# Kernel tuning notes

Hardware: AMD Instinct MI355X
Metric: run time of the kernel (lower is better)

Reference implementation:

```python
import jax, jax.numpy as jnp
import numpy as np

TAU = 1.0
M_OUT = 32  # max_out_node_size
NEG = -1e30


def setup_inputs() -> dict:
    key = jax.random.key(0)
    B, H, U, maxN = 64, 512, 512, 512
    M = M_OUT
    in_size = H + M - 1
    lengths_np = np.where(np.arange(B) % 2 == 0, 256, 512).astype(np.int32)
    total = int(lengths_np.sum())  # 24576
    ks = jax.random.split(key, 14)
    h = jax.random.normal(ks[0], (total, H), jnp.float32)
    hg = jax.random.normal(ks[1], (B, H), jnp.float32)
    u = jax.random.uniform(ks[2], (M, B, maxN), jnp.float32, 1e-20, 1.0)
    gumbel = -jnp.log(-jnp.log(u))
    s = lambda k, shp, fan: jax.random.normal(k, shp, jnp.float32) * (fan ** -0.5)
    return {
        'h': h, 'hg': hg,
        'lengths': jnp.asarray(lengths_np),
        'gumbel': gumbel,
        'W1': s(ks[3], (U, H), H),
        'W2': s(ks[4], (U, H), H),
        'wc': s(ks[5], (U, 1), 1),
        'v': s(ks[6], (1, U), U),
        'w_ih': s(ks[7], (3 * H, in_size), in_size),
        'w_hh': s(ks[8], (3 * H, H), H),
        'b_ih': s(ks[9], (3 * H,), in_size),
        'b_hh': s(ks[10], (3 * H,), in_size),
        'Wf': s(ks[11], (M - 1, H), H),
        'bf': s(ks[12], (M - 1,), H),
    }


def _gru_cell(x, hprev, w_ih, w_hh, b_ih, b_hh):
    H = hprev.shape[-1]
    gi = x @ w_ih.T + b_ih
    gh = hprev @ w_hh.T + b_hh
    r = jax.nn.sigmoid(gi[:, :H] + gh[:, :H])
    z = jax.nn.sigmoid(gi[:, H:2 * H] + gh[:, H:2 * H])
    n = jnp.tanh(gi[:, 2 * H:] + r * gh[:, 2 * H:])
    return (1.0 - z) * n + z * hprev


def reference(h, hg, lengths, gumbel, W1, W2, wc, v, w_ih, w_hh, b_ih, b_hh, Wf, bf):
    B = lengths.shape[0]
    M, _, maxN = gumbel.shape
    H = hg.shape[1]
    total = h.shape[0]
    # pad_sequence: ragged h -> [B, maxN, H], zero-padded
    offsets = jnp.concatenate([jnp.zeros((1,), lengths.dtype), jnp.cumsum(lengths)[:-1]])
    pos = jnp.arange(maxN)
    mask = pos[None, :] < lengths[:, None]                      # [B, maxN]
    idx = jnp.clip(offsets[:, None] + pos[None, :], 0, total - 1)
    enc = h[idx] * mask[..., None].astype(h.dtype)              # [B, maxN, H]
    enc_proj = jnp.einsum('bnh,uh->bnu', enc, W1)               # W1(encoder_out), hoisted
    wc_vec = wc[:, 0]
    v_vec = v[0]
    theta_pos = jnp.arange(M - 1)

    def step(carry, xs):
        dec_in, hid, cov, closs = carry
        g, i = xs
        hid = _gru_cell(dec_in, hid, w_ih, w_hh, b_ih, b_hh)
        uj = jnp.tanh(enc_proj + (hid @ W2.T)[:, None, :] + cov[:, :, None] * wc_vec)
        scores = jnp.einsum('bnu,u->bn', uj, v_vec)
        att = jax.nn.softmax(jnp.where(mask, scores, NEG), axis=-1)  # [B, maxN]
        closs = closs + jnp.minimum(att, cov).sum()
        cov = cov + att
        # gumbel-softmax (hard, straight-through) over nodes
        y = jax.nn.softmax((jnp.log(att + 1e-12) + g) / TAU, axis=1)
        y_hard = jax.nn.one_hot(jnp.argmax(y, axis=1), maxN, dtype=y.dtype)
        att_hard = y_hard + y - jax.lax.stop_gradient(y)
        chosen = jnp.einsum('bnh,bn->bh', enc, att_hard)
        theta = jax.nn.sigmoid(hid @ Wf.T + bf) * (theta_pos < i).astype(hid.dtype)
        dec_in = jnp.concatenate([chosen, theta], axis=1)
        return (dec_in, hid, cov, closs), (att_hard, theta)

    dec_in0 = jnp.zeros((B, H + M - 1), h.dtype)
    cov0 = jnp.zeros((B, maxN), h.dtype)
    carry0 = (dec_in0, hg, cov0, jnp.asarray(0.0, h.dtype))
    (_, _, _, closs), (ptrs, thetas) = jax.lax.scan(step, carry0, (gumbel, jnp.arange(M)))
    pointer = jnp.transpose(ptrs, (1, 2, 0))   # [B, maxN, M]
    adj = jnp.transpose(thetas, (1, 2, 0))     # [B, M-1, M]
    return pointer, closs / B, enc, adj
```

## Files before the change

### kernel.cpp

```cpp
#include <hip/hip_runtime.h>
#include <math.h>

#define B 64
#define H 512
#define MAXN 512
#define U 512
#define MM 32
#define IN_SZ 543
#define DEC_STRIDE 544

#define PTR_OFF 0
#define PTR_SZ (B*MAXN*MM)
#define CLOSS_OFF (PTR_OFF + PTR_SZ)
#define ENC_OFF (CLOSS_OFF + 1)
#define ENC_SZ (B*MAXN*H)
#define ADJ_OFF (ENC_OFF + ENC_SZ)

#define EP_OFF 0
#define EP_SZ (B*MAXN*U)
#define GP_OFF (EP_OFF + EP_SZ)
#define GP_SZ (4*3*B*H)
#define HID0_OFF (GP_OFF + GP_SZ)
#define HID1_OFF (HID0_OFF + B*H)
#define W2H_OFF  (HID1_OFF + B*H)
#define COV_OFF  (W2H_OFF + B*H)
#define SC_OFF   (COV_OFF + B*MAXN)
#define DEC_OFF  (SC_OFF + B*MAXN)
#define CL_OFF   (DEC_OFF + B*DEC_STRIDE)
#define OFFS_OFF (CL_OFF + 64)

__device__ __forceinline__ float tanh_fast(float x){
    float e = __builtin_amdgcn_exp2f(x * 2.885390081777927f);
    return 1.0f - 2.0f * __builtin_amdgcn_rcpf(e + 1.0f);
}

__global__ void k_init(float* __restrict__ ws, float* __restrict__ out,
                       const float* __restrict__ hg, const int* __restrict__ lengths){
    int gid = blockIdx.x*256 + threadIdx.x;
    int nth = gridDim.x*256;
    float* ptr = out + PTR_OFF;
    for (int i=gid;i<PTR_SZ;i+=nth) ptr[i]=0.f;
    float* dec = ws + DEC_OFF;
    for (int i=gid;i<B*DEC_STRIDE;i+=nth) dec[i]=0.f;
    float* cov = ws + COV_OFF;
    float* hid0 = ws + HID0_OFF;
    for (int i=gid;i<B*H;i+=nth){ cov[i]=0.f; hid0[i]=hg[i]; }
    if (gid<64) (ws+CL_OFF)[gid]=0.f;
    if (gid==0){
        int* offs=(int*)(ws+OFFS_OFF); int acc=0;
        for(int b=0;b<B;b++){ offs[b]=acc; acc+=lengths[b]; }
    }
}

__global__ __launch_bounds__(256) void k_gather(const float* __restrict__ h,
        const int* __restrict__ lengths, const float* __restrict__ offs_f,
        float* __restrict__ enc){
    const int* offs = (const int*)offs_f;
    int t = threadIdx.x;
    int row = blockIdx.x*2 + (t>>7);
    int c = (t&127)*4;
    int b = row >> 9, n = row & 511;
    int len = lengths[b];
    float4 v = make_float4(0.f,0.f,0.f,0.f);
    if (n < len){
        const float* p = h + (size_t)(offs[b]+n)*H + c;
        v = *(const float4*)p;
    }
    float* q = enc + (size_t)row*H + c;
    q[0]=v.x; q[1]=v.y; q[2]=v.z; q[3]=v.w;
}

__global__ __launch_bounds__(256) void k_gemm_ep(const float* __restrict__ enc,
        const float* __restrict__ W1, float* __restrict__ ep){
    __shared__ float As[16][132];
    __shared__ float Bs[16][132];
    int tid = threadIdx.x;
    int bm = blockIdx.x >> 2, bn = blockIdx.x & 3;
    int r0 = bm*128, u0 = bn*128;
    int ty = tid >> 4, tx = tid & 15;
    float acc[8][8];
#pragma unroll
    for (int i=0;i<8;i++){
#pragma unroll
        for(int j=0;j<8;j++) acc[i][j]=0.f;
    }
    for (int k0=0;k0<512;k0+=16){
#pragma unroll
        for (int it=0; it<8; ++it){
            int idx = tid + it*256;
            int row = idx >> 4, k = idx & 15;
            As[k][row] = enc[(size_t)(r0+row)*512 + k0 + k];
        }
#pragma unroll
        for (int it=0; it<2; ++it){
            int idx = tid + it*256;
            int nn = idx >> 2, c = idx & 3;
            float4 v = *(const float4*)&W1[(size_t)(u0+nn)*512 + k0 + c*4];
            Bs[c*4+0][nn]=v.x; Bs[c*4+1][nn]=v.y; Bs[c*4+2][nn]=v.z; Bs[c*4+3][nn]=v.w;
        }
        __syncthreads();
#pragma unroll
        for (int k=0;k<16;k++){
            float4 a0 = *(const float4*)&As[k][ty*8];
            float4 a1 = *(const float4*)&As[k][ty*8+4];
            float4 b0 = *(const float4*)&Bs[k][tx*4];
            float4 b1 = *(const float4*)&Bs[k][64+tx*4];
            float a[8]={a0.x,a0.y,a0.z,a0.w,a1.x,a1.y,a1.z,a1.w};
            float bb[8]={b0.x,b0.y,b0.z,b0.w,b1.x,b1.y,b1.z,b1.w};
#pragma unroll
            for(int im=0;im<8;im++){
#pragma unroll
                for(int jn=0;jn<8;jn++) acc[im][jn] += a[im]*bb[jn];
            }
        }
        __syncthreads();
    }
#pragma unroll
    for (int im=0;im<8;im++){
        int r = r0 + ty*8 + im;
        float4 v0 = make_float4(acc[im][0],acc[im][1],acc[im][2],acc[im][3]);
        float4 v1 = make_float4(acc[im][4],acc[im][5],acc[im][6],acc[im][7]);
        *(float4*)&ep[(size_t)r*512 + u0 + tx*4] = v0;
        *(float4*)&ep[(size_t)r*512 + u0 + 64 + tx*4] = v1;
    }
}

__global__ __launch_bounds__(256) void k_gruP(const float* __restrict__ dec_in,
        const float* __restrict__ hid_in,
        const float* __restrict__ w_ih, const float* __restrict__ w_hh,
        float* __restrict__ gp){
    __shared__ float As[64][36];
    __shared__ float Ws[12][36];
    int tid=threadIdx.x, b=tid&63, q=tid>>6;
    int s = blockIdx.x >> 7;
    int h0 = (int)(blockIdx.x & 127) * 4;
    const float* xs; int xstride, kbeg, kend; const float* W; int wstride;
    if (s==0){ xs=dec_in; xstride=DEC_STRIDE; kbeg=0;   kend=288;   W=w_ih; wstride=IN_SZ; }
    else if(s==1){ xs=dec_in; xstride=DEC_STRIDE; kbeg=288; kend=IN_SZ; W=w_ih; wstride=IN_SZ; }
    else if(s==2){ xs=hid_in; xstride=512; kbeg=0;   kend=256; W=w_hh; wstride=512; }
    else         { xs=hid_in; xstride=512; kbeg=256; kend=512; W=w_hh; wstride=512; }
    float a0=0.f,a1=0.f,a2=0.f;
    for (int k0=kbeg; k0<kend; k0+=32){
        for (int it=0;it<2;it++){
            int idx=tid+it*256; int row=idx>>3, c=idx&7; int k=k0+c*4;
            float4 v=make_float4(0.f,0.f,0.f,0.f);
            const float* p=&xs[row*xstride+k];
            if (k+3 < kend) v=*(const float4*)p;
            else { if(k<kend)v.x=p[0]; if(k+1<kend)v.y=p[1]; if(k+2<kend)v.z=p[2]; }
            *(float4*)&As[row][c*4]=v;
        }
        if (tid<96){
            int rr=tid>>3, c=tid&7; int g=rr>>2, qq=rr&3;
            int j=g*512 + h0+qq; int k=k0+c*4;
            float4 v=make_float4(0.f,0.f,0.f,0.f);
            const float* p=&W[(size_t)j*wstride+k];
            if (wstride==512){
                v=*(const float4*)p;
            } else {
                if(k<kend)v.x=p[0]; if(k+1<kend)v.y=p[1];
                if(k+2<kend)v.z=p[2]; if(k+3<kend)v.w=p[3];
            }
            *(float4*)&Ws[rr][c*4]=v;
        }
        __syncthreads();
#pragma unroll
        for (int kk=0;kk<32;kk+=4){
            float4 a=*(const float4*)&As[b][kk];
            float4 w0=*(const float4*)&Ws[q][kk];
            float4 w1=*(const float4*)&Ws[4+q][kk];
            float4 w2=*(const float4*)&Ws[8+q][kk];
            a0 += a.x*w0.x + a.y*w0.y + a.z*w0.z + a.w*w0.w;
            a1 += a.x*w1.x + a.y*w1.y + a.z*w1.z + a.w*w1.w;
            a2 += a.x*w2.x + a.y*w2.y + a.z*w2.z + a.w*w2.w;
        }
        __syncthreads();
    }
    int h = h0 + q;
    gp[((s*3+0)*64+b)*512 + h] = a0;
    gp[((s*3+1)*64+b)*512 + h] = a1;
    gp[((s*3+2)*64+b)*512 + h] = a2;
}

__global__ __launch_bounds__(512) void k_mid(const float* __restrict__ gp,
        const float* __restrict__ hid_in, float* __restrict__ hid_out,
        const float* __restrict__ b_ih, const float* __restrict__ b_hh,
        const float* __restrict__ W2, const float* __restrict__ Wf,
        const float* __restrict__ bf,
        float* __restrict__ w2h, float* __restrict__ dec_in,
        float* __restrict__ adj, int step){
    __shared__ float sH[512];
    int b = blockIdx.x >> 2, uc = blockIdx.x & 3;
    int tid = threadIdx.x;
    {
        int h = tid;
        float gI0 = gp[((0*3+0)*64+b)*512+h] + gp[((1*3+0)*64+b)*512+h];
        float gI1 = gp[((0*3+1)*64+b)*512+h] + gp[((1*3+1)*64+b)*512+h];
        float gI2 = gp[((0*3+2)*64+b)*512+h] + gp[((1*3+2)*64+b)*512+h];
        float gH0 = gp[((2*3+0)*64+b)*512+h] + gp[((3*3+0)*64+b)*512+h];
        float gH1 = gp[((2*3+1)*64+b)*512+h] + gp[((3*3+1)*64+b)*512+h];
        float gH2 = gp[((2*3+2)*64+b)*512+h] + gp[((3*3+2)*64+b)*512+h];
        float gi0=gI0+b_ih[h],     gh0=gH0+b_hh[h];
        float gi1=gI1+b_ih[512+h], gh1=gH1+b_hh[512+h];
        float gi2=gI2+b_ih[1024+h],gh2=gH2+b_hh[1024+h];
        float r=1.f/(1.f+expf(-(gi0+gh0)));
        float z=1.f/(1.f+expf(-(gi1+gh1)));
        float nn=tanhf(gi2 + r*gh2);
        float hv=(1.f-z)*nn + z*hid_in[b*512+h];
        sH[h]=hv;
        if (uc==0) hid_out[b*512+h]=hv;
    }
    __syncthreads();
    int wv=tid>>6, lane=tid&63;
    for (int ul=wv; ul<128; ul+=8){
        int u = uc*128 + ul;
        const float* wr = &W2[(size_t)u*512];
        float acc=0.f;
#pragma unroll
        for (int t=0;t<8;t++){ int k=t*64+lane; acc += wr[k]*sH[k]; }
#pragma unroll
        for (int m=1;m<64;m<<=1) acc += __shfl_xor(acc, m, 64);
        if (lane==0) w2h[b*512+u]=acc;
    }
    if (uc==0){
        for (int ul=wv; ul<31; ul+=8){
            const float* wr = &Wf[(size_t)ul*512];
            float acc=0.f;
#pragma unroll
            for (int t=0;t<8;t++){ int k=t*64+lane; acc += wr[k]*sH[k]; }
#pragma unroll
            for (int m=1;m<64;m<<=1) acc += __shfl_xor(acc, m, 64);
            if (lane==0){
                float th = 1.f/(1.f+expf(-(acc + bf[ul])));
                th = (ul < step) ? th : 0.f;
                dec_in[b*DEC_STRIDE + 512 + ul] = th;
                adj[b*992 + ul*32 + step] = th;
            }
        }
    }
}

__global__ __launch_bounds__(256) void k_scores(const float* __restrict__ ep,
        const float* __restrict__ w2h, const float* __restrict__ cov,
        const float* __restrict__ wc, const float* __restrict__ v,
        const int* __restrict__ lengths, float* __restrict__ sc){
    __shared__ float sW[512], sV[512], sC[512];
    int b = blockIdx.x >> 4, nc = blockIdx.x & 15;
    int len = lengths[b];
    if (nc*32 >= len) return;
    int tid=threadIdx.x;
    for (int idx=tid; idx<384; idx+=256){
        int which = idx>>7, c = (idx&127)*4;
        float4 val;
        if (which==0) val=*(const float4*)&w2h[b*512+c];
        else if (which==1) val=*(const float4*)&v[c];
        else val=*(const float4*)&wc[c];
        float* dst = (which==0)?sW:((which==1)?sV:sC);
        *(float4*)&dst[c]=val;
    }
    __syncthreads();
    int wv=tid>>6, lane=tid&63;
    float4 vv0=*(const float4*)&sV[lane*8], vv1=*(const float4*)&sV[lane*8+4];
    float4 cc0=*(const float4*)&sC[lane*8], cc1=*(const float4*)&sC[lane*8+4];
    float4 ww0=*(const float4*)&sW[lane*8], ww1=*(const float4*)&sW[lane*8+4];
#pragma unroll
    for (int r=0;r<8;r++){
        int n = nc*32 + wv*8 + r;
        float cb = cov[b*512+n];
        const float4* rr = (const float4*)&ep[((size_t)b*512+n)*512 + lane*8];
        float4 e0=rr[0], e1=rr[1];
        float acc;
        acc  = tanh_fast(e0.x + ww0.x + cb*cc0.x)*vv0.x;
        acc += tanh_fast(e0.y + ww0.y + cb*cc0.y)*vv0.y;
        acc += tanh_fast(e0.z + ww0.z + cb*cc0.z)*vv0.z;
        acc += tanh_fast(e0.w + ww0.w + cb*cc0.w)*vv0.w;
        acc += tanh_fast(e1.x + ww1.x + cb*cc1.x)*vv1.x;
        acc += tanh_fast(e1.y + ww1.y + cb*cc1.y)*vv1.y;
        acc += tanh_fast(e1.z + ww1.z + cb*cc1.z)*vv1.z;
        acc += tanh_fast(e1.w + ww1.w + cb*cc1.w)*vv1.w;
#pragma unroll
        for (int m=1;m<64;m<<=1) acc += __shfl_xor(acc, m, 64);
        if (lane==0) sc[b*512+n]=acc;
    }
}

__global__ __launch_bounds__(512) void k_soft(const float* __restrict__ sc,
        const float* __restrict__ gum, const int* __restrict__ lengths,
        const float* __restrict__ enc, float* __restrict__ cov,
        float* __restrict__ dec_in, float* __restrict__ closs_b,
        float* __restrict__ pointer, int step){
    __shared__ float red[512];
    __shared__ int  redi[512];
    int b=blockIdx.x, n=threadIdx.x;
    int len=lengths[b];
    float e = (n<len)? expf(sc[b*512+n]) : 0.f;
    red[n]=e; __syncthreads();
    for(int o=256;o>=1;o>>=1){ if(n<o) red[n]+=red[n+o]; __syncthreads(); }
    float Z=red[0]; __syncthreads();
    float att=e/Z;
    float c=cov[b*512+n];
    red[n]=fminf(att,c); __syncthreads();
    for(int o=256;o>=1;o>>=1){ if(n<o) red[n]+=red[n+o]; __syncthreads(); }
    if(n==0) closs_b[b]+=red[0];
    __syncthreads();
    cov[b*512+n]=c+att;
    float lg=logf(att+1e-12f)+gum[((size_t)step*64+b)*512+n];
    red[n]=lg; redi[n]=n; __syncthreads();
    for(int o=256;o>=1;o>>=1){
        if(n<o && red[n+o]>red[n]){ red[n]=red[n+o]; redi[n]=redi[n+o]; }
        __syncthreads();
    }
    int ns=redi[0];
    if(n==0) pointer[b*16384 + ns*32 + step]=1.f;
    dec_in[b*DEC_STRIDE+n]=enc[((size_t)b*512+ns)*512+n];
}

__global__ void k_final(const float* __restrict__ closs_b, float* __restrict__ out){
    if (threadIdx.x==0 && blockIdx.x==0){
        float s=0.f;
        for(int b=0;b<B;b++) s+=closs_b[b];
        out[CLOSS_OFF]=s/64.f;
    }
}

extern "C" void kernel_launch(void* const* d_in, const int* in_sizes, int n_in,
                              void* d_out, int out_size, void* d_ws, size_t ws_size,
                              hipStream_t stream){
    const float* h      = (const float*)d_in[0];
    const float* hg     = (const float*)d_in[1];
    const int*   lengths= (const int*)  d_in[2];
    const float* gumbel = (const float*)d_in[3];
    const float* W1     = (const float*)d_in[4];
    const float* W2     = (const float*)d_in[5];
    const float* wc     = (const float*)d_in[6];
    const float* v      = (const float*)d_in[7];
    const float* w_ih   = (const float*)d_in[8];
    const float* w_hh   = (const float*)d_in[9];
    const float* b_ih   = (const float*)d_in[10];
    const float* b_hh   = (const float*)d_in[11];
    const float* Wf     = (const float*)d_in[12];
    const float* bf     = (const float*)d_in[13];
    float* out = (float*)d_out;
    float* ws  = (float*)d_ws;
    float* enc = out + ENC_OFF;
    float* adj = out + ADJ_OFF;
    float* pointer = out + PTR_OFF;
    float* ep   = ws + EP_OFF;
    float* gp   = ws + GP_OFF;
    float* hidA = ws + HID0_OFF;
    float* hidB = ws + HID1_OFF;
    float* w2h  = ws + W2H_OFF;
    float* cov  = ws + COV_OFF;
    float* sc   = ws + SC_OFF;
    float* dec  = ws + DEC_OFF;
    float* clb  = ws + CL_OFF;

    hipLaunchKernelGGL(k_init,   dim3(512),  dim3(256), 0, stream, ws, out, hg, lengths);
    hipLaunchKernelGGL(k_gather, dim3(16384),dim3(256), 0, stream, h, lengths, ws+OFFS_OFF, enc);
    hipLaunchKernelGGL(k_gemm_ep,dim3(1024), dim3(256), 0, stream, enc, W1, ep);

    for (int i=0;i<MM;i++){
        const float* hin = (i&1)? hidB : hidA;
        float*       hout= (i&1)? hidA : hidB;
        hipLaunchKernelGGL(k_gruP,   dim3(512),  dim3(256), 0, stream,
                           dec, hin, w_ih, w_hh, gp);
        hipLaunchKernelGGL(k_mid,    dim3(256),  dim3(512), 0, stream,
                           gp, hin, hout, b_ih, b_hh, W2, Wf, bf, w2h, dec, adj, i);
        hipLaunchKernelGGL(k_scores, dim3(1024), dim3(256), 0, stream,
                           ep, w2h, cov, wc, v, lengths, sc);
        hipLaunchKernelGGL(k_soft,   dim3(64),   dim3(512), 0, stream,
                           sc, gumbel, lengths, enc, cov, dec, clb, pointer, i);
    }
    hipLaunchKernelGGL(k_final, dim3(1), dim3(64), 0, stream, clb, out);
}
```

Baseline: 1.848 ms.

## Fuse per-step GRU tail, scoring and softmax into one kernel; MFMA encoder projection

Result: slower. 2.555 ms (+38.2%).

```diff
diff --git a/kernel.cpp b/kernel.cpp
--- a/kernel.cpp
+++ b/kernel.cpp
@@ -22,20 +22,29 @@
 #define GP_SZ (4*3*B*H)
 #define HID0_OFF (GP_OFF + GP_SZ)
 #define HID1_OFF (HID0_OFF + B*H)
-#define W2H_OFF  (HID1_OFF + B*H)
-#define COV_OFF  (W2H_OFF + B*H)
-#define SC_OFF   (COV_OFF + B*MAXN)
-#define DEC_OFF  (SC_OFF + B*MAXN)
+#define COV_OFF  (HID1_OFF + B*H)
+#define DEC_OFF  (COV_OFF + B*MAXN)
 #define CL_OFF   (DEC_OFF + B*DEC_STRIDE)
 #define OFFS_OFF (CL_OFF + 64)
+#define W2T_OFF  (OFFS_OFF + 64)
+
+typedef short bf16x8 __attribute__((ext_vector_type(8)));
+typedef float f32x4  __attribute__((ext_vector_type(4)));
 
 __device__ __forceinline__ float tanh_fast(float x){
     float e = __builtin_amdgcn_exp2f(x * 2.885390081777927f);
     return 1.0f - 2.0f * __builtin_amdgcn_rcpf(e + 1.0f);
 }
 
+__device__ __forceinline__ unsigned short f2bf(float x){
+    unsigned int u = __float_as_uint(x);
+    u = (u + 0x7fffu + ((u >> 16) & 1u)) >> 16;
+    return (unsigned short)u;
+}
+
 __global__ void k_init(float* __restrict__ ws, float* __restrict__ out,
-                       const float* __restrict__ hg, const int* __restrict__ lengths){
+                       const float* __restrict__ hg, const int* __restrict__ lengths,
+                       const float* __restrict__ W2){
     int gid = blockIdx.x*256 + threadIdx.x;
     int nth = gridDim.x*256;
     float* ptr = out + PTR_OFF;
@@ -45,6 +54,11 @@
     float* cov = ws + COV_OFF;
     float* hid0 = ws + HID0_OFF;
     for (int i=gid;i<B*H;i+=nth){ cov[i]=0.f; hid0[i]=hg[i]; }
+    float* w2t = ws + W2T_OFF;
+    for (int i=gid;i<512*512;i+=nth){
+        int u = i >> 9, k = i & 511;
+        w2t[k*512 + u] = W2[i];
+    }
     if (gid<64) (ws+CL_OFF)[gid]=0.f;
     if (gid==0){
         int* offs=(int*)(ws+OFFS_OFF); int acc=0;
@@ -70,58 +84,86 @@
     q[0]=v.x; q[1]=v.y; q[2]=v.z; q[3]=v.w;
 }
 
-__global__ __launch_bounds__(256) void k_gemm_ep(const float* __restrict__ enc,
+__global__ __launch_bounds__(256) void k_gemm_mfma(const float* __restrict__ enc,
         const float* __restrict__ W1, float* __restrict__ ep){
-    __shared__ float As[16][132];
-    __shared__ float Bs[16][132];
+    __shared__ unsigned short sAH[128][40];
+    __shared__ unsigned short sAL[128][40];
+    __shared__ unsigned short sBH[128][40];
+    __shared__ unsigned short sBL[128][40];
     int tid = threadIdx.x;
     int bm = blockIdx.x >> 2, bn = blockIdx.x & 3;
     int r0 = bm*128, u0 = bn*128;
-    int ty = tid >> 4, tx = tid & 15;
-    float acc[8][8];
-#pragma unroll
-    for (int i=0;i<8;i++){
-#pragma unroll
-        for(int j=0;j<8;j++) acc[i][j]=0.f;
-    }
-    for (int k0=0;k0<512;k0+=16){
-#pragma unroll
-        for (int it=0; it<8; ++it){
-            int idx = tid + it*256;
-            int row = idx >> 4, k = idx & 15;
-            As[k][row] = enc[(size_t)(r0+row)*512 + k0 + k];
-        }
-#pragma unroll
-        for (int it=0; it<2; ++it){
-            int idx = tid + it*256;
-            int nn = idx >> 2, c = idx & 3;
-            float4 v = *(const float4*)&W1[(size_t)(u0+nn)*512 + k0 + c*4];
-            Bs[c*4+0][nn]=v.x; Bs[c*4+1][nn]=v.y; Bs[c*4+2][nn]=v.z; Bs[c*4+3][nn]=v.w;
+    int wid = tid>>6, lane = tid&63;
+    int wr = wid>>1, wc = wid&1;
+    int lr = lane&15, lk = (lane>>4)*8;
+    f32x4 acc[4][4];
+#pragma unroll
+    for (int i=0;i<4;i++)
+#pragma unroll
+        for (int j=0;j<4;j++) acc[i][j] = (f32x4){0.f,0.f,0.f,0.f};
+    int rowA = tid>>2, seg = tid&3;
+    for (int k0=0;k0<512;k0+=32){
+#pragma unroll
+        for (int half=0; half<2; ++half){
+            int row = rowA + half*64;
+            const float* asrc = &enc[(size_t)(r0+row)*512 + k0 + seg*8];
+            bf16x8 vh, vl;
+#pragma unroll
+            for (int j=0;j<8;j++){
+                float x = asrc[j];
+                unsigned short hb = f2bf(x);
+                float hf = __uint_as_float(((unsigned int)hb)<<16);
+                vh[j] = (short)hb;
+                vl[j] = (short)f2bf(x - hf);
+            }
+            *(bf16x8*)&sAH[row][seg*8] = vh;
+            *(bf16x8*)&sAL[row][seg*8] = vl;
+            const float* bsrc = &W1[(size_t)(u0+row)*512 + k0 + seg*8];
+            float4 b0 = *(const float4*)bsrc;
+            float4 b1 = *(const float4*)(bsrc+4);
+            float xb[8] = {b0.x,b0.y,b0.z,b0.w,b1.x,b1.y,b1.z,b1.w};
+            bf16x8 wh, wl;
+#pragma unroll
+            for (int j=0;j<8;j++){
+                unsigned short hb = f2bf(xb[j]);
+                float hf = __uint_as_float(((unsigned int)hb)<<16);
+                wh[j] = (short)hb;
+                wl[j] = (short)f2bf(xb[j] - hf);
+            }
+            *(bf16x8*)&sBH[row][seg*8] = wh;
+            *(bf16x8*)&sBL[row][seg*8] = wl;
         }
         __syncthreads();
-#pragma unroll
-        for (int k=0;k<16;k++){
-            float4 a0 = *(const float4*)&As[k][ty*8];
-            float4 a1 = *(const float4*)&As[k][ty*8+4];
-            float4 b0 = *(const float4*)&Bs[k][tx*4];
-            float4 b1 = *(const float4*)&Bs[k][64+tx*4];
-            float a[8]={a0.x,a0.y,a0.z,a0.w,a1.x,a1.y,a1.z,a1.w};
-            float bb[8]={b0.x,b0.y,b0.z,b0.w,b1.x,b1.y,b1.z,b1.w};
-#pragma unroll
-            for(int im=0;im<8;im++){
-#pragma unroll
-                for(int jn=0;jn<8;jn++) acc[im][jn] += a[im]*bb[jn];
+        bf16x8 aH[4], aL[4], bH[4], bL[4];
+#pragma unroll
+        for (int f=0; f<4; f++){
+            aH[f] = *(const bf16x8*)&sAH[wr*64+f*16+lr][lk];
+            aL[f] = *(const bf16x8*)&sAL[wr*64+f*16+lr][lk];
+            bH[f] = *(const bf16x8*)&sBH[wc*64+f*16+lr][lk];
+            bL[f] = *(const bf16x8*)&sBL[wc*64+f*16+lr][lk];
+        }
+#pragma unroll
+        for (int mf=0;mf<4;mf++){
+#pragma unroll
+            for (int nf=0;nf<4;nf++){
+                acc[mf][nf] = __builtin_amdgcn_mfma_f32_16x16x32_bf16(aH[mf], bH[nf], acc[mf][nf], 0,0,0);
+                acc[mf][nf] = __builtin_amdgcn_mfma_f32_16x16x32_bf16(aH[mf], bL[nf], acc[mf][nf], 0,0,0);
+                acc[mf][nf] = __builtin_amdgcn_mfma_f32_16x16x32_bf16(aL[mf], bH[nf], acc[mf][nf], 0,0,0);
             }
         }
         __syncthreads();
     }
 #pragma unroll
-    for (int im=0;im<8;im++){
-        int r = r0 + ty*8 + im;
-        float4 v0 = make_float4(acc[im][0],acc[im][1],acc[im][2],acc[im][3]);
-        float4 v1 = make_float4(acc[im][4],acc[im][5],acc[im][6],acc[im][7]);
-        *(float4*)&ep[(size_t)r*512 + u0 + tx*4] = v0;
-        *(float4*)&ep[(size_t)r*512 + u0 + 64 + tx*4] = v1;
+    for (int mf=0;mf<4;mf++){
+#pragma unroll
+        for (int nf=0;nf<4;nf++){
+#pragma unroll
+            for (int r=0;r<4;r++){
+                int row = r0 + wr*64 + mf*16 + (lane>>4)*4 + r;
+                int col = u0 + wc*64 + nf*16 + lr;
+                ep[(size_t)row*512 + col] = acc[mf][nf][r];
+            }
+        }
     }
 }
 
@@ -181,17 +223,27 @@
     gp[((s*3+2)*64+b)*512 + h] = a2;
 }
 
-__global__ __launch_bounds__(512) void k_mid(const float* __restrict__ gp,
-        const float* __restrict__ hid_in, float* __restrict__ hid_out,
+__global__ __launch_bounds__(1024) void k_ss(
+        const float* __restrict__ gp, const float* __restrict__ hid_in,
+        float* __restrict__ hid_out,
         const float* __restrict__ b_ih, const float* __restrict__ b_hh,
-        const float* __restrict__ W2, const float* __restrict__ Wf,
-        const float* __restrict__ bf,
-        float* __restrict__ w2h, float* __restrict__ dec_in,
+        const float* __restrict__ w2t, const float* __restrict__ Wf,
+        const float* __restrict__ bf_,
+        const float* __restrict__ wc, const float* __restrict__ v,
+        const float* __restrict__ ep, const float* __restrict__ gum,
+        const int* __restrict__ lengths, const float* __restrict__ enc,
+        float* __restrict__ cov, float* __restrict__ dec_in,
+        float* __restrict__ clb, float* __restrict__ pointer,
         float* __restrict__ adj, int step){
-    __shared__ float sH[512];
-    int b = blockIdx.x >> 2, uc = blockIdx.x & 3;
-    int tid = threadIdx.x;
-    {
+    __shared__ float sH[512], sV[512], sC[512], sCov[512];
+    __shared__ float sWa[512], sWb[512], sW[512], sSc[512];
+    __shared__ float red[512];
+    __shared__ int  redi[512];
+    const int b = blockIdx.x, tid = threadIdx.x;
+    const int wv = tid>>6, lane = tid&63;
+    const int len = lengths[b];
+
+    if (tid < 512){
         int h = tid;
         float gI0 = gp[((0*3+0)*64+b)*512+h] + gp[((1*3+0)*64+b)*512+h];
         float gI1 = gp[((0*3+1)*64+b)*512+h] + gp[((1*3+1)*64+b)*512+h];
@@ -199,119 +251,108 @@
         float gH0 = gp[((2*3+0)*64+b)*512+h] + gp[((3*3+0)*64+b)*512+h];
         float gH1 = gp[((2*3+1)*64+b)*512+h] + gp[((3*3+1)*64+b)*512+h];
         float gH2 = gp[((2*3+2)*64+b)*512+h] + gp[((3*3+2)*64+b)*512+h];
-        float gi0=gI0+b_ih[h],     gh0=gH0+b_hh[h];
-        float gi1=gI1+b_ih[512+h], gh1=gH1+b_hh[512+h];
-        float gi2=gI2+b_ih[1024+h],gh2=gH2+b_hh[1024+h];
+        float gi0=gI0+b_ih[h],      gh0=gH0+b_hh[h];
+        float gi1=gI1+b_ih[512+h],  gh1=gH1+b_hh[512+h];
+        float gi2=gI2+b_ih[1024+h], gh2=gH2+b_hh[1024+h];
         float r=1.f/(1.f+expf(-(gi0+gh0)));
         float z=1.f/(1.f+expf(-(gi1+gh1)));
         float nn=tanhf(gi2 + r*gh2);
         float hv=(1.f-z)*nn + z*hid_in[b*512+h];
         sH[h]=hv;
-        if (uc==0) hid_out[b*512+h]=hv;
-    }
-    __syncthreads();
-    int wv=tid>>6, lane=tid&63;
-    for (int ul=wv; ul<128; ul+=8){
-        int u = uc*128 + ul;
-        const float* wr = &W2[(size_t)u*512];
-        float acc=0.f;
-#pragma unroll
-        for (int t=0;t<8;t++){ int k=t*64+lane; acc += wr[k]*sH[k]; }
-#pragma unroll
-        for (int m=1;m<64;m<<=1) acc += __shfl_xor(acc, m, 64);
-        if (lane==0) w2h[b*512+u]=acc;
-    }
-    if (uc==0){
-        for (int ul=wv; ul<31; ul+=8){
-            const float* wr = &Wf[(size_t)ul*512];
-            float acc=0.f;
-#pragma unroll
-            for (int t=0;t<8;t++){ int k=t*64+lane; acc += wr[k]*sH[k]; }
+        hid_out[b*512+h]=hv;
+    } else {
+        int t2 = tid - 512;
+        if (t2 < 128)      *(float4*)&sV[t2*4]         = *(const float4*)&v[t2*4];
+        else if (t2 < 256) *(float4*)&sC[(t2-128)*4]   = *(const float4*)&wc[(t2-128)*4];
+        else if (t2 < 384) *(float4*)&sCov[(t2-256)*4] = *(const float4*)&cov[b*512+(t2-256)*4];
+    }
+    __syncthreads();
+
+    {
+        int u = tid & 511;
+        int kb = (tid < 512) ? 0 : 256;
+        float acc = 0.f;
+#pragma unroll 8
+        for (int k=0;k<256;k++) acc += sH[kb+k] * w2t[(size_t)(kb+k)*512 + u];
+        if (tid < 512) sWa[u]=acc; else sWb[u]=acc;
+    }
+    __syncthreads();
+
+    if (tid < 512) sW[tid] = sWa[tid] + sWb[tid];
+    if (wv == 15){
+        float4 h0 = *(const float4*)&sH[lane*8];
+        float4 h1 = *(const float4*)&sH[lane*8+4];
+        for (int u=0; u<31; ++u){
+            const float4* wr_ = (const float4*)&Wf[(size_t)u*512 + lane*8];
+            float4 w0=wr_[0], w1=wr_[1];
+            float acc = w0.x*h0.x + w0.y*h0.y + w0.z*h0.z + w0.w*h0.w
+                      + w1.x*h1.x + w1.y*h1.y + w1.z*h1.z + w1.w*h1.w;
 #pragma unroll
             for (int m=1;m<64;m<<=1) acc += __shfl_xor(acc, m, 64);
             if (lane==0){
-                float th = 1.f/(1.f+expf(-(acc + bf[ul])));
-                th = (ul < step) ? th : 0.f;
-                dec_in[b*DEC_STRIDE + 512 + ul] = th;
-                adj[b*992 + ul*32 + step] = th;
-            }
-        }
-    }
-}
-
-__global__ __launch_bounds__(256) void k_scores(const float* __restrict__ ep,
-        const float* __restrict__ w2h, const float* __restrict__ cov,
-        const float* __restrict__ wc, const float* __restrict__ v,
-        const int* __restrict__ lengths, float* __restrict__ sc){
-    __shared__ float sW[512], sV[512], sC[512];
-    int b = blockIdx.x >> 4, nc = blockIdx.x & 15;
-    int len = lengths[b];
-    if (nc*32 >= len) return;
-    int tid=threadIdx.x;
-    for (int idx=tid; idx<384; idx+=256){
-        int which = idx>>7, c = (idx&127)*4;
-        float4 val;
-        if (which==0) val=*(const float4*)&w2h[b*512+c];
-        else if (which==1) val=*(const float4*)&v[c];
-        else val=*(const float4*)&wc[c];
-        float* dst = (which==0)?sW:((which==1)?sV:sC);
-        *(float4*)&dst[c]=val;
-    }
-    __syncthreads();
-    int wv=tid>>6, lane=tid&63;
-    float4 vv0=*(const float4*)&sV[lane*8], vv1=*(const float4*)&sV[lane*8+4];
-    float4 cc0=*(const float4*)&sC[lane*8], cc1=*(const float4*)&sC[lane*8+4];
-    float4 ww0=*(const float4*)&sW[lane*8], ww1=*(const float4*)&sW[lane*8+4];
-#pragma unroll
-    for (int r=0;r<8;r++){
-        int n = nc*32 + wv*8 + r;
-        float cb = cov[b*512+n];
-        const float4* rr = (const float4*)&ep[((size_t)b*512+n)*512 + lane*8];
-        float4 e0=rr[0], e1=rr[1];
-        float acc;
-        acc  = tanh_fast(e0.x + ww0.x + cb*cc0.x)*vv0.x;
-        acc += tanh_fast(e0.y + ww0.y + cb*cc0.y)*vv0.y;
-        acc += tanh_fast(e0.z + ww0.z + cb*cc0.z)*vv0.z;
-        acc += tanh_fast(e0.w + ww0.w + cb*cc0.w)*vv0.w;
-        acc += tanh_fast(e1.x + ww1.x + cb*cc1.x)*vv1.x;
-        acc += tanh_fast(e1.y + ww1.y + cb*cc1.y)*vv1.y;
-        acc += tanh_fast(e1.z + ww1.z + cb*cc1.z)*vv1.z;
-        acc += tanh_fast(e1.w + ww1.w + cb*cc1.w)*vv1.w;
-#pragma unroll
-        for (int m=1;m<64;m<<=1) acc += __shfl_xor(acc, m, 64);
-        if (lane==0) sc[b*512+n]=acc;
-    }
-}
-
-__global__ __launch_bounds__(512) void k_soft(const float* __restrict__ sc,
-        const float* __restrict__ gum, const int* __restrict__ lengths,
-        const float* __restrict__ enc, float* __restrict__ cov,
-        float* __restrict__ dec_in, float* __restrict__ closs_b,
-        float* __restrict__ pointer, int step){
-    __shared__ float red[512];
-    __shared__ int  redi[512];
-    int b=blockIdx.x, n=threadIdx.x;
-    int len=lengths[b];
-    float e = (n<len)? expf(sc[b*512+n]) : 0.f;
-    red[n]=e; __syncthreads();
-    for(int o=256;o>=1;o>>=1){ if(n<o) red[n]+=red[n+o]; __syncthreads(); }
-    float Z=red[0]; __syncthreads();
-    float att=e/Z;
-    float c=cov[b*512+n];
-    red[n]=fminf(att,c); __syncthreads();
-    for(int o=256;o>=1;o>>=1){ if(n<o) red[n]+=red[n+o]; __syncthreads(); }
-    if(n==0) closs_b[b]+=red[0];
-    __syncthreads();
-    cov[b*512+n]=c+att;
-    float lg=logf(att+1e-12f)+gum[((size_t)step*64+b)*512+n];
-    red[n]=lg; redi[n]=n; __syncthreads();
-    for(int o=256;o>=1;o>>=1){
-        if(n<o && red[n+o]>red[n]){ red[n]=red[n+o]; redi[n]=redi[n+o]; }
+                float th = 1.f/(1.f+expf(-(acc + bf_[u])));
+                th = (u < step) ? th : 0.f;
+                dec_in[b*DEC_STRIDE + 512 + u] = th;
+                adj[b*992 + u*32 + step] = th;
+            }
+        }
+    }
+    __syncthreads();
+
+    {
+        float4 vv0=*(const float4*)&sV[lane*8], vv1=*(const float4*)&sV[lane*8+4];
+        float4 cc0=*(const float4*)&sC[lane*8], cc1=*(const float4*)&sC[lane*8+4];
+        float4 ww0=*(const float4*)&sW[lane*8], ww1=*(const float4*)&sW[lane*8+4];
+        for (int n=wv; n<len; n+=16){
+            float cb = sCov[n];
+            const float4* rr = (const float4*)&ep[((size_t)b*512+n)*512 + lane*8];
+            float4 e0=rr[0], e1=rr[1];
+            float acc;
+            acc  = tanh_fast(e0.x + ww0.x + cb*cc0.x)*vv0.x;
+            acc += tanh_fast(e0.y + ww0.y + cb*cc0.y)*vv0.y;
+            acc += tanh_fast(e0.z + ww0.z + cb*cc0.z)*vv0.z;
+            acc += tanh_fast(e0.w + ww0.w + cb*cc0.w)*vv0.w;
+            acc += tanh_fast(e1.x + ww1.x + cb*cc1.x)*vv1.x;
+            acc += tanh_fast(e1.y + ww1.y + cb*cc1.y)*vv1.y;
+            acc += tanh_fast(e1.z + ww1.z + cb*cc1.z)*vv1.z;
+            acc += tanh_fast(e1.w + ww1.w + cb*cc1.w)*vv1.w;
+#pragma unroll
+            for (int m=1;m<64;m<<=1) acc += __shfl_xor(acc, m, 64);
+            if (lane==0) sSc[n]=acc;
+        }
+    }
+    __syncthreads();
+
+    int n = tid;
+    float e = 0.f;
+    if (n < 512){ e = (n < len) ? expf(sSc[n]) : 0.f; red[n] = e; }
+    __syncthreads();
+    for (int o=256;o>=1;o>>=1){ if (n<o) red[n]+=red[n+o]; __syncthreads(); }
+    float Z = red[0];
+    __syncthreads();
+    float att = 0.f, cvo = 0.f;
+    if (n < 512){
+        att = e / Z;
+        cvo = sCov[n];
+        red[n] = fminf(att, cvo);
+    }
+    __syncthreads();
+    for (int o=256;o>=1;o>>=1){ if (n<o) red[n]+=red[n+o]; __syncthreads(); }
+    if (tid==0) clb[b] += red[0];
+    __syncthreads();
+    if (n < 512){
+        cov[b*512+n] = cvo + att;
+        float lg = logf(att + 1e-12f) + gum[((size_t)step*64+b)*512 + n];
+        red[n] = lg; redi[n] = n;
+    }
+    __syncthreads();
+    for (int o=256;o>=1;o>>=1){
+        if (n<o && red[n+o]>red[n]){ red[n]=red[n+o]; redi[n]=redi[n+o]; }
         __syncthreads();
     }
-    int ns=redi[0];
-    if(n==0) pointer[b*16384 + ns*32 + step]=1.f;
-    dec_in[b*DEC_STRIDE+n]=enc[((size_t)b*512+ns)*512+n];
+    int ns = redi[0];
+    if (tid==0) pointer[b*16384 + ns*32 + step] = 1.f;
+    if (n < 512) dec_in[b*DEC_STRIDE + n] = enc[((size_t)b*512+ns)*512 + n];
 }
 
 __global__ void k_final(const float* __restrict__ closs_b, float* __restrict__ out){
@@ -348,27 +389,23 @@
     float* gp   = ws + GP_OFF;
     float* hidA = ws + HID0_OFF;
     float* hidB = ws + HID1_OFF;
-    float* w2h  = ws + W2H_OFF;
     float* cov  = ws + COV_OFF;
-    float* sc   = ws + SC_OFF;
     float* dec  = ws + DEC_OFF;
     float* clb  = ws + CL_OFF;
-
-    hipLaunchKernelGGL(k_init,   dim3(512),  dim3(256), 0, stream, ws, out, hg, lengths);
-    hipLaunchKernelGGL(k_gather, dim3(16384),dim3(256), 0, stream, h, lengths, ws+OFFS_OFF, enc);
-    hipLaunchKernelGGL(k_gemm_ep,dim3(1024), dim3(256), 0, stream, enc, W1, ep);
+    float* w2t  = ws + W2T_OFF;
+
+    hipLaunchKernelGGL(k_init,     dim3(512),  dim3(256), 0, stream, ws, out, hg, lengths, W2);
+    hipLaunchKernelGGL(k_gather,   dim3(16384),dim3(256), 0, stream, h, lengths, ws+OFFS_OFF, enc);
+    hipLaunchKernelGGL(k_gemm_mfma,dim3(1024), dim3(256), 0, stream, enc, W1, ep);
 
     for (int i=0;i<MM;i++){
         const float* hin = (i&1)? hidB : hidA;
         float*       hout= (i&1)? hidA : hidB;
-        hipLaunchKernelGGL(k_gruP,   dim3(512),  dim3(256), 0, stream,
+        hipLaunchKernelGGL(k_gruP, dim3(512), dim3(256), 0, stream,
                            dec, hin, w_ih, w_hh, gp);
-        hipLaunchKernelGGL(k_mid,    dim3(256),  dim3(512), 0, stream,
-                           gp, hin, hout, b_ih, b_hh, W2, Wf, bf, w2h, dec, adj, i);
-        hipLaunchKernelGGL(k_scores, dim3(1024), dim3(256), 0, stream,
-                           ep, w2h, cov, wc, v, lengths, sc);
-        hipLaunchKernelGGL(k_soft,   dim3(64),   dim3(512), 0, stream,
-                           sc, gumbel, lengths, enc, cov, dec, clb, pointer, i);
+        hipLaunchKernelGGL(k_ss,   dim3(64),  dim3(1024), 0, stream,
+                           gp, hin, hout, b_ih, b_hh, w2t, Wf, bf, wc, v,
+                           ep, gumbel, lengths, enc, cov, dec, clb, pointer, adj, i);
     }
     hipLaunchKernelGGL(k_final, dim3(1), dim3(64), 0, stream, clb, out);
 }
```

## Compute encoder projection GEMM with split-bf16 MFMA instead of FP32 FMA

Applied to the files above, without the earlier changes.

After: 1.732 ms. 1.07x faster.

```diff
diff --git a/kernel.cpp b/kernel.cpp
--- a/kernel.cpp
+++ b/kernel.cpp
@@ -28,14 +28,26 @@
 #define DEC_OFF  (SC_OFF + B*MAXN)
 #define CL_OFF   (DEC_OFF + B*DEC_STRIDE)
 #define OFFS_OFF (CL_OFF + 64)
+#define W1H_OFF  (OFFS_OFF + 64)
+#define W1L_OFF  (W1H_OFF + 131072)
+
+typedef short bf16x8 __attribute__((ext_vector_type(8)));
+typedef float f32x4  __attribute__((ext_vector_type(4)));
 
 __device__ __forceinline__ float tanh_fast(float x){
     float e = __builtin_amdgcn_exp2f(x * 2.885390081777927f);
     return 1.0f - 2.0f * __builtin_amdgcn_rcpf(e + 1.0f);
 }
 
+__device__ __forceinline__ unsigned short f2bf(float x){
+    unsigned int u = __float_as_uint(x);
+    u = (u + 0x7fffu + ((u >> 16) & 1u)) >> 16;
+    return (unsigned short)u;
+}
+
 __global__ void k_init(float* __restrict__ ws, float* __restrict__ out,
-                       const float* __restrict__ hg, const int* __restrict__ lengths){
+                       const float* __restrict__ hg, const int* __restrict__ lengths,
+                       const float* __restrict__ W1){
     int gid = blockIdx.x*256 + threadIdx.x;
     int nth = gridDim.x*256;
     float* ptr = out + PTR_OFF;
@@ -45,6 +57,15 @@
     float* cov = ws + COV_OFF;
     float* hid0 = ws + HID0_OFF;
     for (int i=gid;i<B*H;i+=nth){ cov[i]=0.f; hid0[i]=hg[i]; }
+    unsigned short* w1h = (unsigned short*)(ws + W1H_OFF);
+    unsigned short* w1l = (unsigned short*)(ws + W1L_OFF);
+    for (int i=gid;i<512*512;i+=nth){
+        float x = W1[i];
+        unsigned short hb = f2bf(x);
+        float hf = __uint_as_float(((unsigned int)hb)<<16);
+        w1h[i] = hb;
+        w1l[i] = f2bf(x - hf);
+    }
     if (gid<64) (ws+CL_OFF)[gid]=0.f;
     if (gid==0){
         int* offs=(int*)(ws+OFFS_OFF); int acc=0;
@@ -70,58 +91,76 @@
     q[0]=v.x; q[1]=v.y; q[2]=v.z; q[3]=v.w;
 }
 
-__global__ __launch_bounds__(256) void k_gemm_ep(const float* __restrict__ enc,
-        const float* __restrict__ W1, float* __restrict__ ep){
-    __shared__ float As[16][132];
-    __shared__ float Bs[16][132];
+__global__ __launch_bounds__(256) void k_gemm_mfma(const float* __restrict__ enc,
+        const unsigned short* __restrict__ w1h, const unsigned short* __restrict__ w1l,
+        float* __restrict__ ep){
+    __shared__ unsigned short sAH[128][40];
+    __shared__ unsigned short sAL[128][40];
+    __shared__ unsigned short sBH[128][40];
+    __shared__ unsigned short sBL[128][40];
     int tid = threadIdx.x;
     int bm = blockIdx.x >> 2, bn = blockIdx.x & 3;
     int r0 = bm*128, u0 = bn*128;
-    int ty = tid >> 4, tx = tid & 15;
-    float acc[8][8];
-#pragma unroll
-    for (int i=0;i<8;i++){
-#pragma unroll
-        for(int j=0;j<8;j++) acc[i][j]=0.f;
-    }
-    for (int k0=0;k0<512;k0+=16){
-#pragma unroll
-        for (int it=0; it<8; ++it){
-            int idx = tid + it*256;
-            int row = idx >> 4, k = idx & 15;
-            As[k][row] = enc[(size_t)(r0+row)*512 + k0 + k];
-        }
-#pragma unroll
-        for (int it=0; it<2; ++it){
-            int idx = tid + it*256;
-            int nn = idx >> 2, c = idx & 3;
-            float4 v = *(const float4*)&W1[(size_t)(u0+nn)*512 + k0 + c*4];
-            Bs[c*4+0][nn]=v.x; Bs[c*4+1][nn]=v.y; Bs[c*4+2][nn]=v.z; Bs[c*4+3][nn]=v.w;
+    int wid = tid>>6, lane = tid&63;
+    int wr = wid>>1, wc = wid&1;
+    int lr = lane&15, lk = (lane>>4)*8;
+    f32x4 acc[4][4];
+#pragma unroll
+    for (int i=0;i<4;i++)
+#pragma unroll
+        for (int j=0;j<4;j++) acc[i][j] = (f32x4){0.f,0.f,0.f,0.f};
+    int rowA = tid>>2, seg = tid&3;
+    for (int k0=0;k0<512;k0+=32){
+#pragma unroll
+        for (int half=0; half<2; ++half){
+            int row = rowA + half*64;
+            const float* asrc = &enc[(size_t)(r0+row)*512 + k0 + seg*8];
+            bf16x8 vh, vl;
+#pragma unroll
+            for (int j=0;j<8;j++){
+                float x = asrc[j];
+                unsigned short hb = f2bf(x);
+                float hf = __uint_as_float(((unsigned int)hb)<<16);
+                vh[j] = (short)hb;
+                vl[j] = (short)f2bf(x - hf);
+            }
+            *(bf16x8*)&sAH[row][seg*8] = vh;
+            *(bf16x8*)&sAL[row][seg*8] = vl;
+            size_t bidx = (size_t)(u0+row)*512 + k0 + seg*8;
+            *(bf16x8*)&sBH[row][seg*8] = *(const bf16x8*)&w1h[bidx];
+            *(bf16x8*)&sBL[row][seg*8] = *(const bf16x8*)&w1l[bidx];
         }
         __syncthreads();
-#pragma unroll
-        for (int k=0;k<16;k++){
-            float4 a0 = *(const float4*)&As[k][ty*8];
-            float4 a1 = *(const float4*)&As[k][ty*8+4];
-            float4 b0 = *(const float4*)&Bs[k][tx*4];
-            float4 b1 = *(const float4*)&Bs[k][64+tx*4];
-            float a[8]={a0.x,a0.y,a0.z,a0.w,a1.x,a1.y,a1.z,a1.w};
-            float bb[8]={b0.x,b0.y,b0.z,b0.w,b1.x,b1.y,b1.z,b1.w};
-#pragma unroll
-            for(int im=0;im<8;im++){
-#pragma unroll
-                for(int jn=0;jn<8;jn++) acc[im][jn] += a[im]*bb[jn];
+        bf16x8 aH[4], aL[4], bH[4], bL[4];
+#pragma unroll
+        for (int f=0; f<4; f++){
+            aH[f] = *(const bf16x8*)&sAH[wr*64+f*16+lr][lk];
+            aL[f] = *(const bf16x8*)&sAL[wr*64+f*16+lr][lk];
+            bH[f] = *(const bf16x8*)&sBH[wc*64+f*16+lr][lk];
+            bL[f] = *(const bf16x8*)&sBL[wc*64+f*16+lr][lk];
+        }
+#pragma unroll
+        for (int mf=0;mf<4;mf++){
+#pragma unroll
+            for (int nf=0;nf<4;nf++){
+                acc[mf][nf] = __builtin_amdgcn_mfma_f32_16x16x32_bf16(aH[mf], bH[nf], acc[mf][nf], 0,0,0);
+                acc[mf][nf] = __builtin_amdgcn_mfma_f32_16x16x32_bf16(aH[mf], bL[nf], acc[mf][nf], 0,0,0);
+                acc[mf][nf] = __builtin_amdgcn_mfma_f32_16x16x32_bf16(aL[mf], bH[nf], acc[mf][nf], 0,0,0);
             }
         }
         __syncthreads();
     }
 #pragma unroll
-    for (int im=0;im<8;im++){
-        int r = r0 + ty*8 + im;
-        float4 v0 = make_float4(acc[im][0],acc[im][1],acc[im][2],acc[im][3]);
-        float4 v1 = make_float4(acc[im][4],acc[im][5],acc[im][6],acc[im][7]);
-        *(float4*)&ep[(size_t)r*512 + u0 + tx*4] = v0;
-        *(float4*)&ep[(size_t)r*512 + u0 + 64 + tx*4] = v1;
+    for (int mf=0;mf<4;mf++){
+#pragma unroll
+        for (int nf=0;nf<4;nf++){
+#pragma unroll
+            for (int r=0;r<4;r++){
+                int row = r0 + wr*64 + mf*16 + (lane>>4)*4 + r;
+                int col = u0 + wc*64 + nf*16 + lr;
+                ep[(size_t)row*512 + col] = acc[mf][nf][r];
+            }
+        }
     }
 }
 
@@ -353,10 +392,12 @@
     float* sc   = ws + SC_OFF;
     float* dec  = ws + DEC_OFF;
     float* clb  = ws + CL_OFF;
-
-    hipLaunchKernelGGL(k_init,   dim3(512),  dim3(256), 0, stream, ws, out, hg, lengths);
-    hipLaunchKernelGGL(k_gather, dim3(16384),dim3(256), 0, stream, h, lengths, ws+OFFS_OFF, enc);
-    hipLaunchKernelGGL(k_gemm_ep,dim3(1024), dim3(256), 0, stream, enc, W1, ep);
+    const unsigned short* w1h = (const unsigned short*)(ws + W1H_OFF);
+    const unsigned short* w1l = (const unsigned short*)(ws + W1L_OFF);
+
+    hipLaunchKernelGGL(k_init,     dim3(512),  dim3(256), 0, stream, ws, out, hg, lengths, W1);
+    hipLaunchKernelGGL(k_gather,   dim3(16384),dim3(256), 0, stream, h, lengths, ws+OFFS_OFF, enc);
+    hipLaunchKernelGGL(k_gemm_mfma,dim3(1024), dim3(256), 0, stream, enc, w1h, w1l, ep);
 
     for (int i=0;i<MM;i++){
         const float* hin = (i&1)? hidB : hidA;
```
